# Performance work log

Measured on AMD Instinct MI355X. Metric: run time of the kernel, lower is better.

The kernel has to match this reference:

```python
import jax, jax.numpy as jnp
import numpy as np

N_LAYERS = 3  # config['lightGCN_n_layers']


def spmm(row, col, val, x, n):
    # sparse COO (row, col, val) @ dense x  ->  [n, d]
    return jax.ops.segment_sum(val[:, None] * x[col], row, num_segments=n)


def setup_inputs() -> dict:
    key = jax.random.key(0)
    ku, ki, kr, kc, kv = jax.random.split(key, 5)
    n_users, n_items, d, n_edges = 75000, 75000, 64, 3_000_000
    n = n_users + n_items
    # nn.init.normal_(std=0.1) embedding init
    user_emb = jax.random.normal(ku, (n_users, d), jnp.float32) * 0.1
    item_emb = jax.random.normal(ki, (n_items, d), jnp.float32) * 0.1
    edge_row = jax.random.randint(kr, (n_edges,), 0, n)
    edge_col = jax.random.randint(kc, (n_edges,), 0, n)
    # normalized adjacency values (D^-1/2 A D^-1/2); ~1/deg scale so propagation stays bounded
    edge_val = jax.random.uniform(kv, (n_edges,), jnp.float32) / 20.0
    return {"user_emb": user_emb, "item_emb": item_emb,
            "edge_row": edge_row, "edge_col": edge_col, "edge_val": edge_val}


def reference(user_emb, item_emb, edge_row, edge_col, edge_val):
    # LightGCN.computer1 (eval path, no edge dropout)
    n_users = user_emb.shape[0]
    all_emb = jnp.concatenate([user_emb, item_emb], axis=0)  # [N, D]
    n = all_emb.shape[0]
    embs = [all_emb]
    for _ in range(N_LAYERS):
        all_emb = spmm(edge_row, edge_col, edge_val, all_emb, n)
        embs.append(all_emb)
    embs = jnp.stack(embs, axis=1)          # [N, L+1, D]
    light_out = jnp.mean(embs, axis=1)      # [N, D]
    users = light_out[:n_users]
    items = light_out[n_users:]
    return users, items, embs
```

## Files before the change

### kernel.cpp

```cpp
#include <hip/hip_runtime.h>
#include <hip/hip_fp16.h>

#define D 64
#define TILE 4096
#define BKSHIFT 9
#define NBKMAX 512
#define COLBITS 18
#define COLMASK ((1 << COLBITS) - 1)
#define SCHUNK 2048

__device__ __forceinline__ unsigned h2_as_u(__half2 h) { return *reinterpret_cast<unsigned*>(&h); }
__device__ __forceinline__ __half2 u_as_h2(unsigned u) { return *reinterpret_cast<__half2*>(&u); }

__global__ void init_emb_kernel(const float4* __restrict__ ue, const float4* __restrict__ ie,
                                float4* __restrict__ embs, __half* __restrict__ xh,
                                int n_users, int n) {
    int idx  = blockIdx.x * blockDim.x + threadIdx.x;
    int node = idx >> 4, q = idx & 15;
    if (node >= n) return;
    float4 v = (node < n_users) ? ue[node * 16 + q] : ie[(node - n_users) * 16 + q];
    embs[(size_t)node * 64 + q] = v;
    if (xh) {
        uint2 o;
        o.x = h2_as_u(__floats2half2_rn(v.x, v.y));
        o.y = h2_as_u(__floats2half2_rn(v.z, v.w));
        ((uint2*)(xh + (size_t)node * 64))[q] = o;
    }
}

__global__ void passA_kernel(const int* __restrict__ row, int* __restrict__ hm,
                             int m, int ntiles, int nbk) {
    __shared__ int h[NBKMAX];
    int t = threadIdx.x;
    for (int b = t; b < nbk; b += 256) h[b] = 0;
    __syncthreads();
    int base = blockIdx.x * TILE;
    for (int k = 0; k < TILE; k += 256) {
        int i = base + k + t;
        if (i < m) atomicAdd(&h[row[i] >> BKSHIFT], 1);
    }
    __syncthreads();
    for (int b = t; b < nbk; b += 256) hm[b * ntiles + blockIdx.x] = h[b];
}

__global__ void passB1_kernel(const int* __restrict__ hm, int* __restrict__ bsums, int len) {
    __shared__ int s[256];
    int t = threadIdx.x;
    int base = blockIdx.x * SCHUNK;
    int sum = 0;
#pragma unroll
    for (int k = 0; k < SCHUNK; k += 256) {
        int i = base + k + t;
        if (i < len) sum += hm[i];
    }
    s[t] = sum;
    __syncthreads();
    for (int d = 128; d > 0; d >>= 1) {
        if (t < d) s[t] += s[t + d];
        __syncthreads();
    }
    if (t == 0) bsums[blockIdx.x] = s[0];
}

__global__ void __launch_bounds__(1024) passB2_kernel(int* __restrict__ bsums,
                                                      int* __restrict__ bstart,
                                                      int* __restrict__ offs_n,
                                                      int nblk, int total, int nbk) {
    __shared__ int s[1024];
    int t = threadIdx.x;
    int v = (t < nblk) ? bsums[t] : 0;
    s[t] = v;
    for (int d = 1; d < 1024; d <<= 1) {
        __syncthreads();
        int add = (t >= d) ? s[t - d] : 0;
        __syncthreads();
        s[t] += add;
    }
    __syncthreads();
    if (t < nblk) bsums[t] = s[t] - v;
    if (t == 0) { bstart[nbk] = total; offs_n[0] = total; }
}

__global__ void passB3_kernel(int* __restrict__ hm, const int* __restrict__ bsums,
                              int* __restrict__ bstart, int len, int ntiles) {
    __shared__ int s[SCHUNK];
    __shared__ int ts[256];
    int t = threadIdx.x;
    int base = blockIdx.x * SCHUNK;
#pragma unroll
    for (int k = 0; k < SCHUNK; k += 256) {
        int i = base + k + t;
        s[k + t] = (i < len) ? hm[i] : 0;
    }
    __syncthreads();
    const int PT = SCHUNK / 256;
    int o = t * PT;
    int sum = 0;
#pragma unroll
    for (int k = 0; k < PT; ++k) sum += s[o + k];
    ts[t] = sum;
    for (int d = 1; d < 256; d <<= 1) {
        __syncthreads();
        int add = (t >= d) ? ts[t - d] : 0;
        __syncthreads();
        ts[t] += add;
    }
    __syncthreads();
    int run = bsums[blockIdx.x] + ts[t] - sum;
#pragma unroll
    for (int k = 0; k < PT; ++k) {
        int v = s[o + k];
        s[o + k] = run;
        run += v;
    }
    __syncthreads();
#pragma unroll
    for (int k = 0; k < SCHUNK; k += 256) {
        int i = base + k + t;
        if (i < len) {
            int pv = s[k + t];
            hm[i] = pv;
            if (i % ntiles == 0) bstart[i / ntiles] = pv;
        }
    }
}

__global__ void __launch_bounds__(1024) passB_kernel(int* __restrict__ hm,
                                                     int* __restrict__ bstart,
                                                     int* __restrict__ offs_n,
                                                     int total, int len, int ntiles, int nbk) {
    __shared__ int s[1024];
    int t = threadIdx.x;
    int chunk = (len + 1023) / 1024;
    int beg = t * chunk;
    int end = beg + chunk; if (end > len) end = len; if (beg > len) beg = len;
    int sum = 0;
    for (int i = beg; i < end; ++i) sum += hm[i];
    s[t] = sum;
    for (int d = 1; d < 1024; d <<= 1) {
        __syncthreads();
        int add = (t >= d) ? s[t - d] : 0;
        __syncthreads();
        s[t] += add;
    }
    __syncthreads();
    int run = s[t] - sum;
    for (int i = beg; i < end; ++i) {
        int v = hm[i];
        hm[i] = run;
        if (i % ntiles == 0) bstart[i / ntiles] = run;
        run += v;
    }
    if (t == 0) { bstart[nbk] = total; offs_n[0] = total; }
}

__global__ void passC_kernel(const int* __restrict__ row, const int* __restrict__ col,
                             const float* __restrict__ val, const int* __restrict__ hm,
                             int2* __restrict__ bcv, int m, int ntiles, int nbk) {
    __shared__ int cur[NBKMAX];
    int t = threadIdx.x;
    for (int b = t; b < nbk; b += 256) cur[b] = hm[b * ntiles + blockIdx.x];
    __syncthreads();
    int base = blockIdx.x * TILE;
    for (int k = 0; k < TILE; k += 256) {
        int i = base + k + t;
        if (i < m) {
            int r = row[i];
            int dst = atomicAdd(&cur[r >> BKSHIFT], 1);
            bcv[dst] = make_int2(col[i] | ((r & ((1 << BKSHIFT) - 1)) << COLBITS),
                                 __float_as_int(val[i]));
        }
    }
}

__global__ void __launch_bounds__(512) pass2_kernel(const int2* __restrict__ bcv,
                                                    const int* __restrict__ bstart,
                                                    int* __restrict__ offs,
                                                    int2* __restrict__ cedges, int n) {
    __shared__ int hist[1 << BKSHIFT];
    __shared__ int s[1 << BKSHIFT];
    int b = blockIdx.x;
    int t = threadIdx.x;
    int e0 = bstart[b], e1 = bstart[b + 1];
    hist[t] = 0;
    __syncthreads();
    for (int i = e0 + t; i < e1; i += 512)
        atomicAdd(&hist[((unsigned)bcv[i].x) >> COLBITS], 1);
    __syncthreads();
    int v = hist[t];
    s[t] = v;
    for (int d = 1; d < 512; d <<= 1) {
        __syncthreads();
        int add = (t >= d) ? s[t - d] : 0;
        __syncthreads();
        s[t] += add;
    }
    __syncthreads();
    int abs_off = e0 + s[t] - v;
    int grow = (b << BKSHIFT) + t;
    if (grow < n) offs[grow] = abs_off;
    __syncthreads();
    hist[t] = abs_off;
    __syncthreads();
    for (int i = e0 + t; i < e1; i += 512) {
        int2 e = bcv[i];
        unsigned u = (unsigned)e.x;
        int pos = atomicAdd(&hist[u >> COLBITS], 1);
        cedges[pos] = make_int2((int)(u & COLMASK), e.y);
    }
}

__global__ void hist_kernel(const int* __restrict__ row, int* __restrict__ counts, int m) {
    int i = blockIdx.x * blockDim.x + threadIdx.x;
    if (i < m) atomicAdd(&counts[row[i]], 1);
}
__global__ void blocksum_kernel(const int* __restrict__ counts, int* __restrict__ bsum, int n) {
    __shared__ int s[256];
    int t = threadIdx.x;
    int i = blockIdx.x * 256 + t;
    s[t] = (i < n) ? counts[i] : 0;
    __syncthreads();
    for (int d = 128; d > 0; d >>= 1) {
        if (t < d) s[t] += s[t + d];
        __syncthreads();
    }
    if (t == 0) bsum[blockIdx.x] = s[0];
}
__global__ void scanb_kernel(const int* __restrict__ bsum, int* __restrict__ boff, int nb) {
    __shared__ int s[1024];
    int t = threadIdx.x;
    int v = (t < nb) ? bsum[t] : 0;
    s[t] = v;
    for (int d = 1; d < 1024; d <<= 1) {
        __syncthreads();
        int add = (t >= d) ? s[t - d] : 0;
        __syncthreads();
        s[t] += add;
    }
    __syncthreads();
    if (t < nb) boff[t] = s[t] - v;
}
__global__ void final_kernel(int* __restrict__ offs, int* __restrict__ cursors,
                             const int* __restrict__ boff, int n, int total) {
    __shared__ int s[256];
    int t = threadIdx.x;
    int i = blockIdx.x * 256 + t;
    int v = (i < n) ? offs[i] : 0;
    s[t] = v;
    for (int d = 1; d < 256; d <<= 1) {
        __syncthreads();
        int add = (t >= d) ? s[t - d] : 0;
        __syncthreads();
        s[t] += add;
    }
    __syncthreads();
    int excl = s[t] - v + boff[blockIdx.x];
    if (i < n) { offs[i] = excl; cursors[i] = excl; }
    if (i == 0) offs[n] = total;
}
__global__ void scatter_kernel(const int* __restrict__ row, const int* __restrict__ col,
                               const float* __restrict__ val, int* __restrict__ cursors,
                               int2* __restrict__ edges, int m) {
    int i = blockIdx.x * blockDim.x + threadIdx.x;
    if (i >= m) return;
    int r   = row[i];
    int pos = atomicAdd(&cursors[r], 1);
    edges[pos] = make_int2(col[i], __float_as_int(val[i]));
}

__global__ void __launch_bounds__(256) spmm_h_kernel(const int* __restrict__ offs,
                                                     const int2* __restrict__ edges,
                                                     const __half* __restrict__ xh,
                                                     float* __restrict__ y,
                                                     __half* __restrict__ yh, int n) {
    int wid  = (int)((blockIdx.x * (size_t)blockDim.x + threadIdx.x) >> 6);
    if (wid >= n) return;
    int lane = threadIdx.x & 63;
    int eg   = lane >> 4;
    int c    = lane & 15;
    int beg = offs[wid], end = offs[wid + 1];
    float4 acc = make_float4(0.f, 0.f, 0.f, 0.f);
    int nfull = (end - beg) & ~3;
    int j = beg;
#pragma unroll 4
    for (; j < beg + nfull; j += 4) {
        int2 e = edges[j + eg];
        float v = __int_as_float(e.y);
        uint2 u = ((const uint2*)(xh + (size_t)e.x * 64))[c];
        float2 f0 = __half22float2(u_as_h2(u.x));
        float2 f1 = __half22float2(u_as_h2(u.y));
        acc.x += v * f0.x; acc.y += v * f0.y; acc.z += v * f1.x; acc.w += v * f1.y;
    }
    if (j + eg < end) {
        int2 e = edges[j + eg];
        float v = __int_as_float(e.y);
        uint2 u = ((const uint2*)(xh + (size_t)e.x * 64))[c];
        float2 f0 = __half22float2(u_as_h2(u.x));
        float2 f1 = __half22float2(u_as_h2(u.y));
        acc.x += v * f0.x; acc.y += v * f0.y; acc.z += v * f1.x; acc.w += v * f1.y;
    }
    acc.x += __shfl_xor(acc.x, 16); acc.y += __shfl_xor(acc.y, 16);
    acc.z += __shfl_xor(acc.z, 16); acc.w += __shfl_xor(acc.w, 16);
    acc.x += __shfl_xor(acc.x, 32); acc.y += __shfl_xor(acc.y, 32);
    acc.z += __shfl_xor(acc.z, 32); acc.w += __shfl_xor(acc.w, 32);
    if (eg == 0) {
        ((float4*)(y + (size_t)wid * 256))[c] = acc;
        uint2 o;
        o.x = h2_as_u(__floats2half2_rn(acc.x, acc.y));
        o.y = h2_as_u(__floats2half2_rn(acc.z, acc.w));
        ((uint2*)(yh + (size_t)wid * 64))[c] = o;
    }
}

__global__ void __launch_bounds__(256) spmm_mean_h_kernel(const int* __restrict__ offs,
                                                          const int2* __restrict__ edges,
                                                          const __half* __restrict__ xh,
                                                          float* __restrict__ y,
                                                          const float4* __restrict__ embs,
                                                          float4* __restrict__ users,
                                                          float4* __restrict__ items,
                                                          int n_users, int n) {
    int wid  = (int)((blockIdx.x * (size_t)blockDim.x + threadIdx.x) >> 6);
    if (wid >= n) return;
    int lane = threadIdx.x & 63;
    int eg   = lane >> 4;
    int c    = lane & 15;
    int beg = offs[wid], end = offs[wid + 1];
    float4 acc = make_float4(0.f, 0.f, 0.f, 0.f);
    int nfull = (end - beg) & ~3;
    int j = beg;
#pragma unroll 4
    for (; j < beg + nfull; j += 4) {
        int2 e = edges[j + eg];
        float v = __int_as_float(e.y);
        uint2 u = ((const uint2*)(xh + (size_t)e.x * 64))[c];
        float2 f0 = __half22float2(u_as_h2(u.x));
        float2 f1 = __half22float2(u_as_h2(u.y));
        acc.x += v * f0.x; acc.y += v * f0.y; acc.z += v * f1.x; acc.w += v * f1.y;
    }
    if (j + eg < end) {
        int2 e = edges[j + eg];
        float v = __int_as_float(e.y);
        uint2 u = ((const uint2*)(xh + (size_t)e.x * 64))[c];
        float2 f0 = __half22float2(u_as_h2(u.x));
        float2 f1 = __half22float2(u_as_h2(u.y));
        acc.x += v * f0.x; acc.y += v * f0.y; acc.z += v * f1.x; acc.w += v * f1.y;
    }
    acc.x += __shfl_xor(acc.x, 16); acc.y += __shfl_xor(acc.y, 16);
    acc.z += __shfl_xor(acc.z, 16); acc.w += __shfl_xor(acc.w, 16);
    acc.x += __shfl_xor(acc.x, 32); acc.y += __shfl_xor(acc.y, 32);
    acc.z += __shfl_xor(acc.z, 32); acc.w += __shfl_xor(acc.w, 32);
    if (eg == 0) {
        ((float4*)(y + (size_t)wid * 256))[c] = acc;
        const float4* p = embs + (size_t)wid * 64 + c;
        float4 a = p[0], b = p[16], d = p[32];
        float4 mv;
        mv.x = (a.x + b.x + d.x + acc.x) * 0.25f;
        mv.y = (a.y + b.y + d.y + acc.y) * 0.25f;
        mv.z = (a.z + b.z + d.z + acc.z) * 0.25f;
        mv.w = (a.w + b.w + d.w + acc.w) * 0.25f;
        if (wid < n_users) users[wid * 16 + c] = mv;
        else               items[(wid - n_users) * 16 + c] = mv;
    }
}

__global__ void __launch_bounds__(256) spmm_kernel(const int* __restrict__ offs,
                                                   const int2* __restrict__ edges,
                                                   const float* __restrict__ x,
                                                   float* __restrict__ y, int n) {
    int wid  = (int)((blockIdx.x * (size_t)blockDim.x + threadIdx.x) >> 6);
    if (wid >= n) return;
    int lane = threadIdx.x & 63;
    int eg   = lane >> 4;
    int c    = lane & 15;
    int beg = offs[wid], end = offs[wid + 1];
    float4 acc = make_float4(0.f, 0.f, 0.f, 0.f);
    int nfull = (end - beg) & ~3;
    int j = beg;
#pragma unroll 4
    for (; j < beg + nfull; j += 4) {
        int2 e = edges[j + eg];
        float v = __int_as_float(e.y);
        float4 xv = ((const float4*)(x + (size_t)e.x * 256))[c];
        acc.x += v * xv.x; acc.y += v * xv.y; acc.z += v * xv.z; acc.w += v * xv.w;
    }
    if (j + eg < end) {
        int2 e = edges[j + eg];
        float v = __int_as_float(e.y);
        float4 xv = ((const float4*)(x + (size_t)e.x * 256))[c];
        acc.x += v * xv.x; acc.y += v * xv.y; acc.z += v * xv.z; acc.w += v * xv.w;
    }
    acc.x += __shfl_xor(acc.x, 16); acc.y += __shfl_xor(acc.y, 16);
    acc.z += __shfl_xor(acc.z, 16); acc.w += __shfl_xor(acc.w, 16);
    acc.x += __shfl_xor(acc.x, 32); acc.y += __shfl_xor(acc.y, 32);
    acc.z += __shfl_xor(acc.z, 32); acc.w += __shfl_xor(acc.w, 32);
    if (eg == 0)
        ((float4*)(y + (size_t)wid * 256))[c] = acc;
}

__global__ void __launch_bounds__(256) spmm_mean_kernel(const int* __restrict__ offs,
                                                        const int2* __restrict__ edges,
                                                        const float* __restrict__ x,
                                                        float* __restrict__ y,
                                                        const float4* __restrict__ embs,
                                                        float4* __restrict__ users,
                                                        float4* __restrict__ items,
                                                        int n_users, int n) {
    int wid  = (int)((blockIdx.x * (size_t)blockDim.x + threadIdx.x) >> 6);
    if (wid >= n) return;
    int lane = threadIdx.x & 63;
    int eg   = lane >> 4;
    int c    = lane & 15;
    int beg = offs[wid], end = offs[wid + 1];
    float4 acc = make_float4(0.f, 0.f, 0.f, 0.f);
    int nfull = (end - beg) & ~3;
    int j = beg;
#pragma unroll 4
    for (; j < beg + nfull; j += 4) {
        int2 e = edges[j + eg];
        float v = __int_as_float(e.y);
        float4 xv = ((const float4*)(x + (size_t)e.x * 256))[c];
        acc.x += v * xv.x; acc.y += v * xv.y; acc.z += v * xv.z; acc.w += v * xv.w;
    }
    if (j + eg < end) {
        int2 e = edges[j + eg];
        float v = __int_as_float(e.y);
        float4 xv = ((const float4*)(x + (size_t)e.x * 256))[c];
        acc.x += v * xv.x; acc.y += v * xv.y; acc.z += v * xv.z; acc.w += v * xv.w;
    }
    acc.x += __shfl_xor(acc.x, 16); acc.y += __shfl_xor(acc.y, 16);
    acc.z += __shfl_xor(acc.z, 16); acc.w += __shfl_xor(acc.w, 16);
    acc.x += __shfl_xor(acc.x, 32); acc.y += __shfl_xor(acc.y, 32);
    acc.z += __shfl_xor(acc.z, 32); acc.w += __shfl_xor(acc.w, 32);
    if (eg == 0) {
        ((float4*)(y + (size_t)wid * 256))[c] = acc;
        const float4* p = embs + (size_t)wid * 64 + c;
        float4 a = p[0], b = p[16], d = p[32];
        float4 mv;
        mv.x = (a.x + b.x + d.x + acc.x) * 0.25f;
        mv.y = (a.y + b.y + d.y + acc.y) * 0.25f;
        mv.z = (a.z + b.z + d.z + acc.z) * 0.25f;
        mv.w = (a.w + b.w + d.w + acc.w) * 0.25f;
        if (wid < n_users) users[wid * 16 + c] = mv;
        else               items[(wid - n_users) * 16 + c] = mv;
    }
}

extern "C" void kernel_launch(void* const* d_in, const int* in_sizes, int n_in,
                              void* d_out, int out_size, void* d_ws, size_t ws_size,
                              hipStream_t stream) {
    const float* user_emb = (const float*)d_in[0];
    const float* item_emb = (const float*)d_in[1];
    const int*   edge_row = (const int*)d_in[2];
    const int*   edge_col = (const int*)d_in[3];
    const float* edge_val = (const float*)d_in[4];

    const int n_users = in_sizes[0] / D;
    const int n_items = in_sizes[1] / D;
    const int n       = n_users + n_items;
    const int m       = in_sizes[2];

    float* out_users = (float*)d_out;
    float* out_items = out_users + (size_t)n_users * D;
    float* embs      = out_items + (size_t)n_items * D;

    const int ntiles = (m + TILE - 1) / TILE;
    const int nbk    = (n + (1 << BKSHIFT) - 1) >> BKSHIFT;
    const int nb     = (n + 255) / 256;
    const int len    = nbk * ntiles;
    const int nblk   = (len + SCHUNK - 1) / SCHUNK;

    const size_t xh_bytes = (size_t)n * 128;
    size_t xregion = 2 * xh_bytes;
    if (xregion < (size_t)m * sizeof(int2)) xregion = (size_t)m * sizeof(int2);

    char* ws = (char*)d_ws;
    size_t off = 0;
    int2* cedges = (int2*)(ws + off); off += (size_t)m * sizeof(int2);
    char* X      = ws + off;          off += xregion;
    int*  offs   = (int*)(ws + off);  off += (size_t)(n + 1) * sizeof(int);
    int*  bstart = (int*)(ws + off);  off += (size_t)(nbk + 1) * sizeof(int);
    int*  hm     = (int*)(ws + off);  off += (size_t)nbk * ntiles * sizeof(int);
    int*  cursors= (int*)(ws + off);  off += (size_t)n * sizeof(int);
    int*  bsum   = (int*)(ws + off);  off += (size_t)nb * sizeof(int);
    int*  boff   = (int*)(ws + off);  off += (size_t)nb * sizeof(int);
    bool fp16path = (ws_size >= off);

    if (!fp16path) {
        off = 0;
        cedges = (int2*)(ws + off); off += (size_t)m * sizeof(int2);
        X      = ws + off;          off += (size_t)m * sizeof(int2);
        offs   = (int*)(ws + off);  off += (size_t)(n + 1) * sizeof(int);
        bstart = (int*)(ws + off);  off += (size_t)(nbk + 1) * sizeof(int);
        hm     = (int*)(ws + off);  off += (size_t)nbk * ntiles * sizeof(int);
        cursors= (int*)(ws + off);  off += (size_t)n * sizeof(int);
        bsum   = (int*)(ws + off);  off += (size_t)nb * sizeof(int);
        boff   = (int*)(ws + off);  off += (size_t)nb * sizeof(int);
    }
    int2*   bcv  = (int2*)X;
    __half* xh_a = (__half*)X;
    __half* xh_b = (__half*)(X + xh_bytes);
    const bool radix = (ws_size >= off) && (n <= (1 << COLBITS)) && (nbk <= NBKMAX);

    if (radix) {
        passA_kernel<<<ntiles, 256, 0, stream>>>(edge_row, hm, m, ntiles, nbk);
        if (nblk <= 1024) {
            passB1_kernel<<<nblk, 256, 0, stream>>>(hm, bsum, len);
            passB2_kernel<<<1, 1024, 0, stream>>>(bsum, bstart, offs + n, nblk, m, nbk);
            passB3_kernel<<<nblk, 256, 0, stream>>>(hm, bsum, bstart, len, ntiles);
        } else {
            passB_kernel<<<1, 1024, 0, stream>>>(hm, bstart, offs + n, m,
                                                 len, ntiles, nbk);
        }
        passC_kernel<<<ntiles, 256, 0, stream>>>(edge_row, edge_col, edge_val, hm,
                                                 bcv, m, ntiles, nbk);
        pass2_kernel<<<nbk, 512, 0, stream>>>(bcv, bstart, offs, cedges, n);
    } else {
        hipMemsetAsync(offs, 0, (size_t)n * sizeof(int), stream);
        hist_kernel<<<(m + 255) / 256, 256, 0, stream>>>(edge_row, offs, m);
        blocksum_kernel<<<nb, 256, 0, stream>>>(offs, bsum, n);
        scanb_kernel<<<1, 1024, 0, stream>>>(bsum, boff, nb);
        final_kernel<<<nb, 256, 0, stream>>>(offs, cursors, boff, n, m);
        scatter_kernel<<<(m + 255) / 256, 256, 0, stream>>>(
            edge_row, edge_col, edge_val, cursors, cedges, m);
    }

    init_emb_kernel<<<(n * 16 + 255) / 256, 256, 0, stream>>>(
        (const float4*)user_emb, (const float4*)item_emb, (float4*)embs,
        fp16path ? xh_a : (__half*)nullptr, n_users, n);

    if (fp16path) {
        spmm_h_kernel<<<(n + 3) / 4, 256, 0, stream>>>(offs, cedges, xh_a,
                                                       embs + (size_t)1 * D, xh_b, n);
        spmm_h_kernel<<<(n + 3) / 4, 256, 0, stream>>>(offs, cedges, xh_b,
                                                       embs + (size_t)2 * D, xh_a, n);
        spmm_mean_h_kernel<<<(n + 3) / 4, 256, 0, stream>>>(offs, cedges, xh_a,
                                                            embs + (size_t)3 * D,
                                                            (const float4*)embs,
                                                            (float4*)out_users,
                                                            (float4*)out_items,
                                                            n_users, n);
    } else {
        spmm_kernel<<<(n + 3) / 4, 256, 0, stream>>>(offs, cedges,
                                                     embs + (size_t)0 * D,
                                                     embs + (size_t)1 * D, n);
        spmm_kernel<<<(n + 3) / 4, 256, 0, stream>>>(offs, cedges,
                                                     embs + (size_t)1 * D,
                                                     embs + (size_t)2 * D, n);
        spmm_mean_kernel<<<(n + 3) / 4, 256, 0, stream>>>(offs, cedges,
                                                          embs + (size_t)2 * D,
                                                          embs + (size_t)3 * D,
                                                          (const float4*)embs,
                                                          (float4*)out_users,
                                                          (float4*)out_items,
                                                          n_users, n);
    }
}
```

Baseline: 566.7 us.

## Stage bucket scatter through shared-memory local sort for coalesced global writes

```diff
diff --git a/kernel.cpp b/kernel.cpp
--- a/kernel.cpp
+++ b/kernel.cpp
@@ -154,22 +154,66 @@
     if (t == 0) { bstart[nbk] = total; offs_n[0] = total; }
 }
 
-__global__ void passC_kernel(const int* __restrict__ row, const int* __restrict__ col,
-                             const float* __restrict__ val, const int* __restrict__ hm,
-                             int2* __restrict__ bcv, int m, int ntiles, int nbk) {
-    __shared__ int cur[NBKMAX];
-    int t = threadIdx.x;
-    for (int b = t; b < nbk; b += 256) cur[b] = hm[b * ntiles + blockIdx.x];
-    __syncthreads();
-    int base = blockIdx.x * TILE;
-    for (int k = 0; k < TILE; k += 256) {
-        int i = base + k + t;
+__global__ void __launch_bounds__(256) passC_kernel(const int* __restrict__ row,
+                                                    const int* __restrict__ col,
+                                                    const float* __restrict__ val,
+                                                    const int* __restrict__ hm,
+                                                    int2* __restrict__ bcv,
+                                                    int m, int ntiles, int nbk) {
+    __shared__ int  lh[NBKMAX];
+    __shared__ int  lscan[NBKMAX];
+    __shared__ int  gbase[NBKMAX];
+    __shared__ int  ts[256];
+    __shared__ int2 se[TILE];
+    __shared__ unsigned short sbk[TILE];
+    int t = threadIdx.x;
+    int tile = blockIdx.x;
+    for (int b = t; b < NBKMAX; b += 256) lh[b] = 0;
+    for (int b = t; b < nbk; b += 256) gbase[b] = hm[b * ntiles + tile];
+    __syncthreads();
+    int base = tile * TILE;
+    int cnt  = m - base; if (cnt > TILE) cnt = TILE;
+    int ecol[16], eval_[16], erank[16], ebkt[16];
+#pragma unroll
+    for (int k = 0; k < 16; ++k) {
+        int i = base + k * 256 + t;
+        ebkt[k] = -1;
         if (i < m) {
             int r = row[i];
-            int dst = atomicAdd(&cur[r >> BKSHIFT], 1);
-            bcv[dst] = make_int2(col[i] | ((r & ((1 << BKSHIFT) - 1)) << COLBITS),
-                                 __float_as_int(val[i]));
+            int b = r >> BKSHIFT;
+            ecol[k]  = col[i] | ((r & ((1 << BKSHIFT) - 1)) << COLBITS);
+            eval_[k] = __float_as_int(val[i]);
+            erank[k] = atomicAdd(&lh[b], 1);
+            ebkt[k]  = b;
         }
+    }
+    __syncthreads();
+    int a0 = lh[2 * t], a1 = lh[2 * t + 1];
+    int s2 = a0 + a1;
+    ts[t] = s2;
+    for (int d = 1; d < 256; d <<= 1) {
+        __syncthreads();
+        int add = (t >= d) ? ts[t - d] : 0;
+        __syncthreads();
+        ts[t] += add;
+    }
+    __syncthreads();
+    int ebase = ts[t] - s2;
+    lscan[2 * t]     = ebase;
+    lscan[2 * t + 1] = ebase + a0;
+    __syncthreads();
+#pragma unroll
+    for (int k = 0; k < 16; ++k) {
+        if (ebkt[k] >= 0) {
+            int slot = lscan[ebkt[k]] + erank[k];
+            se[slot]  = make_int2(ecol[k], eval_[k]);
+            sbk[slot] = (unsigned short)ebkt[k];
+        }
+    }
+    __syncthreads();
+    for (int p = t; p < cnt; p += 256) {
+        int b = sbk[p];
+        bcv[gbase[b] + (p - lscan[b])] = se[p];
     }
 }
 
```

Measured after the change: 538.6 us. 5.0% less time.
